# Performance work log

Hardware: AMD Instinct MI355X
Metric: run time of the kernel (lower is better)

## Reference

```python
import jax, jax.numpy as jnp
import numpy as np

N, D, H, O, E, TOP_K = 8192, 1024, 2048, 1024, 8, 2


def setup_inputs() -> dict:
    key = jax.random.key(0)
    ks = jax.random.split(key, 8)
    s = lambda fan: 1.0 / np.sqrt(fan)
    return {
        "x": jax.random.normal(ks[0], (N, D), jnp.float32),
        "W1": jax.random.normal(ks[1], (E, D, H), jnp.float32) * s(D),
        "b1": jnp.zeros((E, H), jnp.float32),
        "W2": jax.random.normal(ks[2], (E, H, H), jnp.float32) * s(H),
        "b2": jnp.zeros((E, H), jnp.float32),
        "W3": jax.random.normal(ks[3], (E, H, O), jnp.float32) * s(H),
        "b3": jnp.zeros((E, O), jnp.float32),
        "Wg1": jax.random.normal(ks[4], (D, 64), jnp.float32) * s(D),
        "bg1": jnp.zeros((64,), jnp.float32),
        "Wg2": jax.random.normal(ks[5], (64, E), jnp.float32) * s(64),
        "bg2": jnp.zeros((E,), jnp.float32),
        "top_k": TOP_K,
    }


def reference(x, W1, b1, W2, b2, W3, b3, Wg1, bg1, Wg2, bg2, top_k):
    # Gating network: Linear -> relu -> Linear -> softmax over experts
    gates = jax.nn.softmax(jax.nn.relu(x @ Wg1 + bg1) @ Wg2 + bg2, axis=1)  # [N, E]
    # Top-k membership mask per token (combine weight is the ORIGINAL gate value,
    # matching the torch code which ignores the renormalized top_k_gates)
    _, top_idx = jax.lax.top_k(gates, top_k)                       # [N, k]
    num_experts = gates.shape[1]
    in_topk = (top_idx[:, :, None] == jnp.arange(num_experts)[None, None, :]).any(axis=1)  # [N, E]
    w = jnp.where(in_topk, gates, 0.0)                             # [N, E]
    # Expert MLPs (dropout is identity at inference). Dense over experts;
    # combine zeros out non-selected experts, matching the masked dispatch math.
    h = jax.nn.relu(jnp.einsum("nd,edh->enh", x, W1) + b1[:, None, :])   # [E, N, H]
    h = jax.nn.relu(jnp.einsum("enh,ehk->enk", h, W2) + b2[:, None, :])  # [E, N, H]
    y = jnp.einsum("enh,eho->eno", h, W3) + b3[:, None, :]               # [E, N, O]
    return jnp.einsum("eno,ne->no", y, w)                                # [N, O]
```

## Files before the change

kernel.cpp:

```cpp
#include <hip/hip_runtime.h>

typedef _Float16 fp16_t;
typedef __attribute__((ext_vector_type(8))) _Float16 f16x8;
typedef __attribute__((ext_vector_type(4))) _Float16 f16x4;
typedef __attribute__((ext_vector_type(4))) float f32x4;

#define N_TOK 8192
#define DIM   1024
#define HID   2048
#define OUTD  1024
#define NE    8
#define NPAIR 16384
#define MAXSLOT 72
#define HBLK 64

__device__ __forceinline__ void load_lds16(const void* g, void* l) {
    __builtin_amdgcn_global_load_lds(
        (__attribute__((address_space(1))) void*)g,
        (__attribute__((address_space(3))) void*)l, 16, 0, 0);
}

__global__ __launch_bounds__(256) void gating_kernel(
    const float* __restrict__ x,  const float* __restrict__ Wg1,
    const float* __restrict__ bg1, const float* __restrict__ Wg2,
    const float* __restrict__ bg2,
    int* __restrict__ top_i, float* __restrict__ top_w)
{
    __shared__ float xs[8][DIM];
    const int tid = threadIdx.x, lane = tid & 63, wv = tid >> 6;

    const float4* x4 = (const float4*)(x + (size_t)blockIdx.x * 8 * DIM);
    float4* xs4 = (float4*)&xs[0][0];
    #pragma unroll
    for (int i = 0; i < 8; ++i) xs4[tid + 256 * i] = x4[tid + 256 * i];
    __syncthreads();

    const int trow = wv * 2;
    const float b = bg1[lane];
    float h00 = b,   h01 = 0.f;
    float h10 = b,   h11 = 0.f;
    for (int d0 = 0; d0 < DIM; d0 += 8) {
        float w[8];
        #pragma unroll
        for (int i = 0; i < 8; ++i) w[i] = Wg1[(d0 + i) * 64 + lane];
        float4 a00 = *(const float4*)&xs[trow][d0];
        float4 a01 = *(const float4*)&xs[trow][d0 + 4];
        float4 a10 = *(const float4*)&xs[trow + 1][d0];
        float4 a11 = *(const float4*)&xs[trow + 1][d0 + 4];
        h00 = fmaf(a00.x, w[0], fmaf(a00.y, w[1], fmaf(a00.z, w[2], fmaf(a00.w, w[3], h00))));
        h01 = fmaf(a01.x, w[4], fmaf(a01.y, w[5], fmaf(a01.z, w[6], fmaf(a01.w, w[7], h01))));
        h10 = fmaf(a10.x, w[0], fmaf(a10.y, w[1], fmaf(a10.z, w[2], fmaf(a10.w, w[3], h10))));
        h11 = fmaf(a11.x, w[4], fmaf(a11.y, w[5], fmaf(a11.z, w[6], fmaf(a11.w, w[7], h11))));
    }
    float hg[2] = { h00 + h01, h10 + h11 };

    #pragma unroll
    for (int t = 0; t < 2; ++t) {
        float h = fmaxf(hg[t], 0.f);
        float p[NE];
        #pragma unroll
        for (int e = 0; e < NE; ++e) p[e] = h * Wg2[lane * NE + e];
        #pragma unroll
        for (int s = 32; s > 0; s >>= 1) {
            #pragma unroll
            for (int e = 0; e < NE; ++e) p[e] += __shfl_xor(p[e], s, 64);
        }
        if (lane == 0) {
            int n = blockIdx.x * 8 + trow + t;
            float g[NE];
            float m = -1e30f;
            #pragma unroll
            for (int e = 0; e < NE; ++e) { g[e] = p[e] + bg2[e]; m = fmaxf(m, g[e]); }
            float s = 0.f;
            #pragma unroll
            for (int e = 0; e < NE; ++e) { g[e] = expf(g[e] - m); s += g[e]; }
            float inv = 1.f / s;
            #pragma unroll
            for (int e = 0; e < NE; ++e) g[e] *= inv;
            int b0 = 0;
            #pragma unroll
            for (int e = 1; e < NE; ++e) if (g[e] > g[b0]) b0 = e;
            int b1 = (b0 == 0) ? 1 : 0;
            #pragma unroll
            for (int e = 0; e < NE; ++e) if (e != b0 && g[e] > g[b1]) b1 = e;
            top_i[n] = b0;          top_i[N_TOK + n] = b1;
            top_w[n] = g[b0];       top_w[N_TOK + n] = g[b1];
        }
    }
}

__global__ __launch_bounds__(256) void hist_kernel(
    const int* __restrict__ top_i, int* __restrict__ blockhist)
{
    __shared__ int wh[4][NE];
    const int tid = threadIdx.x, lane = tid & 63, wv = tid >> 6;
    const int e = top_i[blockIdx.x * 256 + tid];
    #pragma unroll
    for (int e0 = 0; e0 < NE; ++e0) {
        unsigned long long m = __ballot(e == e0);
        if (lane == 0) wh[wv][e0] = __popcll(m);
    }
    __syncthreads();
    if (tid < NE)
        blockhist[blockIdx.x * NE + tid] =
            wh[0][tid] + wh[1][tid] + wh[2][tid] + wh[3][tid];
}

__global__ __launch_bounds__(512) void scan_kernel(
    const int* __restrict__ blockhist, int* __restrict__ offs,
    int* __restrict__ pairbase,
    int* __restrict__ tile_e, int* __restrict__ tile_mt)
{
    __shared__ int h[HBLK * NE], pb[HBLK * NE], off_s[NE + 1];
    const int tid = threadIdx.x;
    h[tid] = blockhist[tid];
    __syncthreads();
    if (tid == 0) {
        int c[NE] = {};
        for (int b = 0; b < HBLK; ++b)
            #pragma unroll
            for (int e = 0; e < NE; ++e) { pb[b * NE + e] = c[e]; c[e] += h[b * NE + e]; }
        int acc = 0;
        #pragma unroll
        for (int e = 0; e < NE; ++e) { off_s[e] = acc; acc += c[e]; }
        off_s[NE] = acc;
        for (int e = 0; e <= NE; ++e) offs[e] = off_s[e];
        int s = 0;
        for (int e = 0; e < NE; ++e) {
            int nt = (c[e] + 255) >> 8;
            for (int mt = 0; mt < nt; ++mt) { tile_e[s] = e; tile_mt[s] = mt; ++s; }
        }
        for (; s < MAXSLOT; ++s) tile_e[s] = -1;
    }
    __syncthreads();
    pairbase[tid] = pb[tid] + off_s[tid & (NE - 1)];
}

__global__ __launch_bounds__(256) void scatter_kernel(
    const int* __restrict__ top_i, const int* __restrict__ pairbase,
    int* __restrict__ pair_token, int* __restrict__ slot)
{
    __shared__ int wh[4][NE];
    const int tid = threadIdx.x, lane = tid & 63, wv = tid >> 6;
    const int p = blockIdx.x * 256 + tid;
    const int e = top_i[p];
    int myrank = 0;
    #pragma unroll
    for (int e0 = 0; e0 < NE; ++e0) {
        unsigned long long m = __ballot(e == e0);
        if (lane == 0) wh[wv][e0] = __popcll(m);
        if (e == e0) myrank = __popcll(m & ((1ull << lane) - 1ull));
    }
    __syncthreads();
    int wprefix = 0;
    for (int w = 0; w < wv; ++w) wprefix += wh[w][e];
    const int pout = pairbase[blockIdx.x * NE + e] + wprefix + myrank;
    pair_token[pout] = p & (N_TOK - 1);
    slot[p] = pout;
}

__global__ __launch_bounds__(256) void xcvt_kernel(
    const float* __restrict__ x, fp16_t* __restrict__ xb)
{
    size_t i = ((size_t)blockIdx.x * 256 + threadIdx.x) * 4;
    float4 v = *(const float4*)(x + i);
    f16x4 o = { (fp16_t)v.x, (fp16_t)v.y, (fp16_t)v.z, (fp16_t)v.w };
    *(f16x4*)(xb + i) = o;
}

__global__ __launch_bounds__(256) void transpose_cvt(
    const float* __restrict__ src, fp16_t* __restrict__ dst, int R, int C)
{
    int bb = blockIdx.z;
    src += (size_t)bb * R * C;
    dst += (size_t)bb * R * C;
    __shared__ float sm[32][33];
    int tx = threadIdx.x & 31, ty = threadIdx.x >> 5;
    int r0 = blockIdx.y * 32, c0 = blockIdx.x * 32;
    #pragma unroll
    for (int i = 0; i < 4; ++i)
        sm[ty + 8 * i][tx] = src[(size_t)(r0 + ty + 8 * i) * C + c0 + tx];
    __syncthreads();
    #pragma unroll
    for (int i = 0; i < 4; ++i)
        dst[(size_t)(c0 + ty + 8 * i) * R + r0 + tx] = (fp16_t)sm[tx][ty + 8 * i];
}

template <int K, int NOUT, bool GATHER, bool RELU, bool OUT_FP16>
__global__ __launch_bounds__(512) void gemm_expert(
    const fp16_t* __restrict__ A, const fp16_t* __restrict__ Wt,
    const float* __restrict__ bias, void* __restrict__ Cout,
    const int* __restrict__ offs, const int* __restrict__ pair_token,
    const int* __restrict__ tile_e, const int* __restrict__ tile_mt)
{
    const int e = tile_e[blockIdx.y];
    if (e < 0) return;
    const int mt  = tile_mt[blockIdx.y];
    const int off = offs[e];
    const int cnt = offs[e + 1] - off;
    const int rows_here = min(256, cnt - mt * 256);
    const int mb = off + mt * 256;
    const int n0 = blockIdx.x * 256;

    extern __shared__ __align__(16) char smem[];

    const int tid = threadIdx.x, lane = tid & 63, wv = tid >> 6;
    const int wm = wv >> 2, wn = wv & 3;
    const int l15 = lane & 15, quad = lane >> 4, sb = l15 & 7;

    const int rowsel = tid >> 3;
    const int coff = ((tid & 7) ^ (rowsel & 7)) * 8;

    const fp16_t* We = Wt + (size_t)e * NOUT * K;

    const fp16_t* aptr[2][2];
    #pragma unroll
    for (int h = 0; h < 2; ++h)
        #pragma unroll
        for (int s = 0; s < 2; ++s) {
            int tr = rowsel + s * 128 + h * 64;
            int rc = (tr < rows_here) ? tr : (rows_here - 1);
            long rowidx = GATHER ? (long)pair_token[mb + rc] : (long)(mb + rc);
            aptr[h][s] = A + rowidx * (long)K + coff;
        }
    const int nbase = (rowsel & 31) + (tid >> 8) * 64;
    const fp16_t* bptr = We + (size_t)(n0 + nbase) * K + coff;

    char* const ldsw = smem + wv * 1024;

#define STAGE_A(h, kt) do {                                                  \
        int _b = ((kt) & 1) * 32768 + (h) * 16384;                           \
        load_lds16(aptr[h][0] + (kt) * 64, ldsw + _b);                       \
        load_lds16(aptr[h][1] + (kt) * 64, ldsw + _b + 8192); } while (0)

#define STAGE_B(h, kt) do {                                                  \
        int _b = 65536 + ((kt) & 1) * 32768 + (h) * 16384;                   \
        load_lds16(bptr + (size_t)((h) * 32) * K + (kt) * 64, ldsw + _b);    \
        load_lds16(bptr + (size_t)((h) * 32 + 128) * K + (kt) * 64,          \
                   ldsw + _b + 8192); } while (0)

    const int slot0 = (quad ^ sb) * 16;
    const int slot1 = ((quad + 4) ^ sb) * 16;
    const int arow = (wm * 64 + l15) * 128;
    const int brow = (wn * 32 + l15) * 128;

    f16x8 a[4][2], b0[2][2], b1[2][2];
    f32x4 acc[8][4] = {};

#define READ_A(buf, h) do {                                                  \
        _Pragma("unroll")                                                    \
        for (int ii = 0; ii < 4; ++ii) {                                     \
            int _b = (buf) * 32768 + (h) * 16384 + arow + ii * 2048;         \
            a[ii][0] = *(const f16x8*)(smem + _b + slot0);                   \
            a[ii][1] = *(const f16x8*)(smem + _b + slot1);                   \
        } } while (0)

#define READ_B(buf, h, br) do {                                              \
        _Pragma("unroll")                                                    \
        for (int jj = 0; jj < 2; ++jj) {                                     \
            int _b = 65536 + (buf) * 32768 + (h) * 16384 + brow + jj * 2048; \
            br[jj][0] = *(const f16x8*)(smem + _b + slot0);                  \
            br[jj][1] = *(const f16x8*)(smem + _b + slot1);                  \
        } } while (0)

#define MFMA_Q(imb, jnb, br) do {                                            \
        _Pragma("unroll")                                                    \
        for (int ks = 0; ks < 2; ++ks)                                       \
        _Pragma("unroll")                                                    \
        for (int ii = 0; ii < 4; ++ii)                                       \
        _Pragma("unroll")                                                    \
        for (int jj = 0; jj < 2; ++jj)                                       \
            acc[(imb) + ii][(jnb) + jj] =                                    \
                __builtin_amdgcn_mfma_f32_16x16x32_f16(                      \
                    a[ii][ks], br[jj][ks], acc[(imb) + ii][(jnb) + jj],      \
                    0, 0, 0); } while (0)

#define BAR() do { asm volatile("" ::: "memory");                            \
                   __builtin_amdgcn_s_barrier();                             \
                   asm volatile("" ::: "memory"); } while (0)
#define LGKM0() asm volatile("s_waitcnt lgkmcnt(0)" ::: "memory")
#define VM6()   asm volatile("s_waitcnt vmcnt(6)" ::: "memory")
#define VM0()   asm volatile("s_waitcnt vmcnt(0)" ::: "memory")

    STAGE_A(0, 0); STAGE_B(0, 0); STAGE_B(1, 0); STAGE_A(1, 0);
    STAGE_A(0, 1); STAGE_B(0, 1); STAGE_B(1, 1);
    VM6();
    BAR();

    const int niter = K / 128;
    for (int i = 0; i < niter; ++i) {
        const int kt0 = 2 * i, kt1 = kt0 + 1;
        const bool pf = (i + 1 < niter);
        READ_A(0, 0); READ_B(0, 0, b0);
        STAGE_A(1, kt1);
        BAR(); LGKM0();
        __builtin_amdgcn_s_setprio(1); MFMA_Q(0, 0, b0); __builtin_amdgcn_s_setprio(0);
        BAR();
        READ_B(0, 1, b1);
        if (pf) STAGE_A(0, kt0 + 2);
        BAR(); LGKM0();
        __builtin_amdgcn_s_setprio(1); MFMA_Q(0, 2, b1); __builtin_amdgcn_s_setprio(0);
        BAR();
        READ_A(0, 1);
        if (pf) STAGE_B(0, kt0 + 2);
        BAR(); LGKM0();
        __builtin_amdgcn_s_setprio(1); MFMA_Q(4, 2, b1); __builtin_amdgcn_s_setprio(0);
        BAR();
        if (pf) STAGE_B(1, kt0 + 2);
        BAR();
        __builtin_amdgcn_s_setprio(1); MFMA_Q(4, 0, b0); __builtin_amdgcn_s_setprio(0);
        if (pf) VM6(); else VM0();
        BAR();
        READ_A(1, 0); READ_B(1, 0, b0);
        if (pf) STAGE_A(1, kt0 + 2);
        BAR(); LGKM0();
        __builtin_amdgcn_s_setprio(1); MFMA_Q(0, 0, b0); __builtin_amdgcn_s_setprio(0);
        BAR();
        READ_B(1, 1, b1);
        if (pf) STAGE_A(0, kt0 + 3);
        BAR(); LGKM0();
        __builtin_amdgcn_s_setprio(1); MFMA_Q(0, 2, b1); __builtin_amdgcn_s_setprio(0);
        BAR();
        READ_A(1, 1);
        if (pf) STAGE_B(0, kt0 + 3);
        BAR(); LGKM0();
        __builtin_amdgcn_s_setprio(1); MFMA_Q(4, 2, b1); __builtin_amdgcn_s_setprio(0);
        BAR();
        if (pf) STAGE_B(1, kt0 + 3);
        BAR();
        __builtin_amdgcn_s_setprio(1); MFMA_Q(4, 0, b0); __builtin_amdgcn_s_setprio(0);
        if (pf) VM6(); else VM0();
        BAR();
    }

#undef STAGE_A
#undef STAGE_B
#undef READ_A
#undef READ_B
#undef MFMA_Q
#undef BAR
#undef LGKM0
#undef VM6
#undef VM0

    const float* be = bias + (size_t)e * NOUT + n0;
    #pragma unroll
    for (int j = 0; j < 4; ++j) {
        int col = wn * 64 + j * 16 + l15;
        float bv = be[col];
        #pragma unroll
        for (int i2 = 0; i2 < 8; ++i2) {
            int mrow0 = wm * 128 + i2 * 16 + quad * 4;
            #pragma unroll
            for (int r = 0; r < 4; ++r) {
                int m = mrow0 + r;
                if (m < rows_here) {
                    float v = acc[i2][j][r] + bv;
                    if (RELU) v = fmaxf(v, 0.f);
                    size_t o = (size_t)(mb + m) * NOUT + n0 + col;
                    if (OUT_FP16) ((fp16_t*)Cout)[o] = (fp16_t)v;
                    else          ((float*)Cout)[o]  = v;
                }
            }
        }
    }
}

__global__ __launch_bounds__(256) void combine_kernel(
    const float* __restrict__ y, const int* __restrict__ slot,
    const float* __restrict__ top_w, float* __restrict__ out)
{
    int idx = blockIdx.x * 256 + threadIdx.x;
    int n  = idx >> 8;
    int o4 = idx & 255;
    int s0 = slot[n], s1 = slot[N_TOK + n];
    float w0 = top_w[n], w1 = top_w[N_TOK + n];
    float4 y0 = *(const float4*)(y + (size_t)s0 * OUTD + o4 * 4);
    float4 y1 = *(const float4*)(y + (size_t)s1 * OUTD + o4 * 4);
    float4 r;
    r.x = w0 * y0.x + w1 * y1.x;
    r.y = w0 * y0.y + w1 * y1.y;
    r.z = w0 * y0.z + w1 * y1.z;
    r.w = w0 * y0.w + w1 * y1.w;
    *(float4*)(out + (size_t)n * OUTD + o4 * 4) = r;
}

extern "C" void kernel_launch(void* const* d_in, const int* in_sizes, int n_in,
                              void* d_out, int out_size, void* d_ws, size_t ws_size,
                              hipStream_t stream)
{
    (void)in_sizes; (void)n_in; (void)out_size; (void)ws_size;
    const float* x   = (const float*)d_in[0];
    const float* W1  = (const float*)d_in[1];
    const float* b1  = (const float*)d_in[2];
    const float* W2  = (const float*)d_in[3];
    const float* b2  = (const float*)d_in[4];
    const float* W3  = (const float*)d_in[5];
    const float* b3  = (const float*)d_in[6];
    const float* Wg1 = (const float*)d_in[7];
    const float* bg1 = (const float*)d_in[8];
    const float* Wg2 = (const float*)d_in[9];
    const float* bg2 = (const float*)d_in[10];

    char* ws = (char*)d_ws;
    fp16_t* xb = (fp16_t*)ws;
    fp16_t* h1 = (fp16_t*)(ws + 16777216);
    fp16_t* h2 = (fp16_t*)(ws + 83886080);
    fp16_t* Wt = (fp16_t*)(ws + 150994944);
    char* rt   = ws + 218103808;
    int*   offs       = (int*)rt;
    int*   tile_e     = offs + 9;
    int*   tile_mt    = tile_e + MAXSLOT;
    int*   top_i      = tile_mt + MAXSLOT;
    float* top_w      = (float*)(top_i + 2 * N_TOK);
    int*   slot       = (int*)(top_w + 2 * N_TOK);
    int*   pair_token = slot + 2 * N_TOK;
    int*   blockhist  = pair_token + NPAIR;
    int*   pairbase   = blockhist + HBLK * NE;

    gating_kernel<<<1024, 256, 0, stream>>>(x, Wg1, bg1, Wg2, bg2, top_i, top_w);
    hist_kernel<<<HBLK, 256, 0, stream>>>(top_i, blockhist);
    scan_kernel<<<1, HBLK * NE, 0, stream>>>(blockhist, offs, pairbase, tile_e, tile_mt);
    scatter_kernel<<<HBLK, 256, 0, stream>>>(top_i, pairbase, pair_token, slot);
    xcvt_kernel<<<8192, 256, 0, stream>>>(x, xb);

    transpose_cvt<<<dim3(HID / 32, DIM / 32, NE), 256, 0, stream>>>(W1, Wt, DIM, HID);
    gemm_expert<DIM, HID, true, true, true>
        <<<dim3(HID / 256, MAXSLOT), 512, 131072, stream>>>(
            xb, Wt, b1, (void*)h1, offs, pair_token, tile_e, tile_mt);

    transpose_cvt<<<dim3(HID / 32, HID / 32, NE), 256, 0, stream>>>(W2, Wt, HID, HID);
    gemm_expert<HID, HID, false, true, true>
        <<<dim3(HID / 256, MAXSLOT), 512, 131072, stream>>>(
            h1, Wt, b2, (void*)h2, offs, pair_token, tile_e, tile_mt);

    transpose_cvt<<<dim3(OUTD / 32, HID / 32, NE), 256, 0, stream>>>(W3, Wt, HID, OUTD);
    gemm_expert<HID, OUTD, false, false, false>
        <<<dim3(OUTD / 256, MAXSLOT), 512, 131072, stream>>>(
            h2, Wt, b3, (void*)h1, offs, pair_token, tile_e, tile_mt);

    combine_kernel<<<8192, 256, 0, stream>>>((const float*)h1, slot, top_w, (float*)d_out);
}
```

Baseline: 858.8 us.

## Remap expert GEMM blocks across XCDs and vectorize fp16 epilogue via LDS

Block indices of the expert GEMM are remapped so that each XCD handles a fixed group of (expert, M-tile) slots, with the N-tiles of one slot placed on the same XCD. The aim is better L2 reuse of the A rows and expert weights. The fp16 output epilogue now stages each 16x64 wave tile through padded LDS and writes 16-byte vector stores instead of scattered 2-byte stores. This adds LDS traffic and assumes the tile table has exactly 72 slots arranged as 8x9 and that the grid dimensions match.

```diff
diff --git a/kernel.cpp b/kernel.cpp
--- a/kernel.cpp
+++ b/kernel.cpp
@@ -193,14 +193,20 @@
     const int* __restrict__ offs, const int* __restrict__ pair_token,
     const int* __restrict__ tile_e, const int* __restrict__ tile_mt)
 {
-    const int e = tile_e[blockIdx.y];
+    const int NX = NOUT / 256;
+    const int L = blockIdx.x + blockIdx.y * NX;
+    const int xcd = L & 7, kk = L >> 3;
+    const int slotI = xcd * 9 + kk % 9;
+    const int ntile = kk / 9;
+
+    const int e = tile_e[slotI];
     if (e < 0) return;
-    const int mt  = tile_mt[blockIdx.y];
+    const int mt  = tile_mt[slotI];
     const int off = offs[e];
     const int cnt = offs[e + 1] - off;
     const int rows_here = min(256, cnt - mt * 256);
     const int mb = off + mt * 256;
-    const int n0 = blockIdx.x * 256;
+    const int n0 = ntile * 256;
 
     extern __shared__ __align__(16) char smem[];
 
@@ -344,22 +350,52 @@
 #undef VM0
 
     const float* be = bias + (size_t)e * NOUT + n0;
-    #pragma unroll
-    for (int j = 0; j < 4; ++j) {
-        int col = wn * 64 + j * 16 + l15;
-        float bv = be[col];
+    float bv[4];
+    #pragma unroll
+    for (int j = 0; j < 4; ++j) bv[j] = be[wn * 64 + j * 16 + l15];
+
+    if (OUT_FP16) {
+        fp16_t* tb = (fp16_t*)(smem + wv * 4096);
+        const int r8 = lane >> 3, c8 = lane & 7;
         #pragma unroll
         for (int i2 = 0; i2 < 8; ++i2) {
-            int mrow0 = wm * 128 + i2 * 16 + quad * 4;
-            #pragma unroll
-            for (int r = 0; r < 4; ++r) {
-                int m = mrow0 + r;
+            #pragma unroll
+            for (int j = 0; j < 4; ++j)
+                #pragma unroll
+                for (int r = 0; r < 4; ++r) {
+                    float v = acc[i2][j][r] + bv[j];
+                    if (RELU) v = fmaxf(v, 0.f);
+                    tb[(quad * 4 + r) * 68 + j * 16 + l15] = (fp16_t)v;
+                }
+            #pragma unroll
+            for (int pass = 0; pass < 2; ++pass) {
+                int row = r8 + pass * 8;
+                f16x4 lo = *(const f16x4*)&tb[row * 68 + c8 * 8];
+                f16x4 hi = *(const f16x4*)&tb[row * 68 + c8 * 8 + 4];
+                int m = wm * 128 + i2 * 16 + row;
                 if (m < rows_here) {
-                    float v = acc[i2][j][r] + bv;
-                    if (RELU) v = fmaxf(v, 0.f);
-                    size_t o = (size_t)(mb + m) * NOUT + n0 + col;
-                    if (OUT_FP16) ((fp16_t*)Cout)[o] = (fp16_t)v;
-                    else          ((float*)Cout)[o]  = v;
+                    f16x8 vv = { lo[0], lo[1], lo[2], lo[3],
+                                 hi[0], hi[1], hi[2], hi[3] };
+                    *(f16x8*)((fp16_t*)Cout + (size_t)(mb + m) * NOUT
+                              + n0 + wn * 64 + c8 * 8) = vv;
+                }
+            }
+        }
+    } else {
+        #pragma unroll
+        for (int j = 0; j < 4; ++j) {
+            int col = wn * 64 + j * 16 + l15;
+            #pragma unroll
+            for (int i2 = 0; i2 < 8; ++i2) {
+                int mrow0 = wm * 128 + i2 * 16 + quad * 4;
+                #pragma unroll
+                for (int r = 0; r < 4; ++r) {
+                    int m = mrow0 + r;
+                    if (m < rows_here) {
+                        float v = acc[i2][j][r] + bv[j];
+                        if (RELU) v = fmaxf(v, 0.f);
+                        ((float*)Cout)[(size_t)(mb + m) * NOUT + n0 + col] = v;
+                    }
                 }
             }
         }
```

Measured after the change: 772.5 us. 1.11x faster.
